# Kernel tuning notes

Hardware: AMD Instinct MI355X
Metric: run time of the kernel (lower is better)

The kernel has to match this reference:

```python
import jax, jax.numpy as jnp
import numpy as np

EMBED_DIM, HIDDEN_DIM, NUM_BINS = 1280, 256, 10

def setup_inputs() -> dict:
    key = jax.random.key(0)
    ks = jax.random.split(key, 7)
    s_in = 1.0 / np.sqrt(EMBED_DIM)
    s_h = 1.0 / np.sqrt(HIDDEN_DIM)
    return {
        "x": jax.random.normal(ks[0], (2, 384, EMBED_DIM), dtype=jnp.float32),
        "Wi": jax.random.uniform(ks[1], (EMBED_DIM, HIDDEN_DIM), jnp.float32, -s_in, s_in),
        "bi": jax.random.uniform(ks[2], (HIDDEN_DIM,), jnp.float32, -s_in, s_in),
        "Wj": jax.random.uniform(ks[3], (EMBED_DIM, HIDDEN_DIM), jnp.float32, -s_in, s_in),
        "bj": jax.random.uniform(ks[4], (HIDDEN_DIM,), jnp.float32, -s_in, s_in),
        "Wo": jax.random.uniform(ks[5], (HIDDEN_DIM, NUM_BINS), jnp.float32, -s_h, s_h),
        "bo": jax.random.uniform(ks[6], (NUM_BINS,), jnp.float32, -s_h, s_h),
    }

def reference(x, Wi, bi, Wj, bj, Wo, bo):
    # x: [B, L, D]
    xi = x @ Wi + bi              # [B, L, H]
    xj = x @ Wj + bj              # [B, L, H]
    pair = xi[:, :, None, :] * xj[:, None, :, :]   # [B, L, L, H]
    h = jax.nn.relu(pair)
    return h @ Wo + bo            # [B, L, L, num_bins]
```

## Files before the change

### kernel.cpp

```cpp
#include <hip/hip_runtime.h>

#define LSEQ 384
#define EMBED 1280
#define HID 256
#define NBINS 10
#define GM 768
#define KP 512

typedef __attribute__((ext_vector_type(8))) short short8;
typedef __attribute__((ext_vector_type(4))) short short4v;
typedef __attribute__((ext_vector_type(4))) float float4v;
typedef __attribute__((ext_vector_type(2))) float float2v;

__device__ __forceinline__ short f2bf(float f) {
    unsigned u = __builtin_bit_cast(unsigned, f);
    u = (u + 0x7fffu + ((u >> 16) & 1u)) >> 16;
    return (short)u;
}

__device__ __forceinline__ void load16_to_lds(const void* g, void* l) {
    __builtin_amdgcn_global_load_lds(
        (const __attribute__((address_space(1))) unsigned int*)g,
        (__attribute__((address_space(3))) unsigned int*)l, 16, 0, 0);
}

__global__ __launch_bounds__(256) void k1_proj_pack(
    const float* __restrict__ x, const float* __restrict__ Wi, const float* __restrict__ bi,
    const float* __restrict__ Wj, const float* __restrict__ bj, const float* __restrict__ Wo,
    short* __restrict__ Aef, short* __restrict__ Bef)
{
    __shared__ short xs[32][32];
    __shared__ short wn[32][32];

    const int tid = threadIdx.x;
    const int m0 = blockIdx.x * 32;
    const int n0 = blockIdx.y * 32;
    const bool isI = (n0 < HID);
    const float* __restrict__ W = isI ? Wi : Wj;
    const int nc0 = n0 & (HID - 1);

    const int lane = tid & 63;
    const int w = tid >> 6;
    const int mh = w >> 1, nh = w & 1;
    const int l15 = lane & 15, q = lane >> 4;

    const int srow = tid >> 3;
    const int sq = (tid & 7) * 4;

    const float* xp = x + (size_t)(m0 + srow) * EMBED + sq;
    const float* wp = W + (size_t)srow * HID + nc0 + sq;

    float4v acc = {0.f, 0.f, 0.f, 0.f};

    for (int ks = 0; ks < EMBED / 32; ++ks) {
        const float4v xv = *(const float4v*)(xp + ks * 32);
        const float4v wv = *(const float4v*)(wp + (size_t)ks * 32 * HID);
        __syncthreads();
        short4v x4;
        x4.x = f2bf(xv.x); x4.y = f2bf(xv.y); x4.z = f2bf(xv.z); x4.w = f2bf(xv.w);
        *(short4v*)&xs[srow][sq] = x4;
        wn[sq + 0][srow] = f2bf(wv.x);
        wn[sq + 1][srow] = f2bf(wv.y);
        wn[sq + 2][srow] = f2bf(wv.z);
        wn[sq + 3][srow] = f2bf(wv.w);
        __syncthreads();
        const short8 a = *(const short8*)&xs[mh * 16 + l15][q * 8];
        const short8 bfr = *(const short8*)&wn[nh * 16 + l15][q * 8];
        acc = __builtin_amdgcn_mfma_f32_16x16x32_bf16(a, bfr, acc, 0, 0, 0);
    }

    const int ncol = n0 + nh * 16 + l15;
    const int mrow0 = m0 + mh * 16;
    if (isI) {
        const int h = ncol;
        float wo[NBINS];
        const float2v* wop = (const float2v*)(Wo + h * NBINS);
#pragma unroll
        for (int c = 0; c < 5; ++c) { float2v t = wop[c]; wo[2 * c] = t.x; wo[2 * c + 1] = t.y; }
        const float bv = bi[h];
#pragma unroll
        for (int r = 0; r < 4; ++r) {
            const int m = mrow0 + q * 4 + r;
            const float v = acc[r] + bv;
            const float p = fmaxf(v, 0.f), pm = fmaxf(-v, 0.f);
            short* ap = Aef + (size_t)m * KP + h;
#pragma unroll
            for (int n = 0; n < NBINS; ++n) {
                ap[(size_t)n * GM * KP]       = f2bf(p  * wo[n]);
                ap[(size_t)n * GM * KP + HID] = f2bf(pm * wo[n]);
            }
        }
    } else {
        const int h = ncol - HID;
        const float bv = bj[h];
#pragma unroll
        for (int r = 0; r < 4; ++r) {
            const int m = mrow0 + q * 4 + r;
            const float v = acc[r] + bv;
            Bef[(size_t)m * KP + h]       = f2bf(fmaxf(v, 0.f));
            Bef[(size_t)m * KP + HID + h] = f2bf(fmaxf(-v, 0.f));
        }
    }
}

__global__ __launch_bounds__(256) void k2_pair_mfma(
    const short* __restrict__ Aef, const short* __restrict__ Bef,
    const float* __restrict__ bo, float* __restrict__ out)
{
    __shared__ __align__(16) char smem[40960];
    short* As = (short*)smem;
    short* Bs = (short*)(smem + 20480);
    float* sout = (float*)smem;

    const int tid = threadIdx.x;
    const int lane = tid & 63;
    const int w = tid >> 6;
    const int ih = w >> 1, jh = w & 1;
    const int l15 = lane & 15, q = lane >> 4;
    const int b = blockIdx.z;
    const int i0 = blockIdx.x * 32, j0 = blockIdx.y * 32;

    const size_t arow0 = (size_t)(b * LSEQ + i0);
    const size_t brow0 = (size_t)(b * LSEQ + j0);
    const int srow = lane >> 2;
    const int skb = (lane & 3) * 8;

    float4v acc[NBINS];
#pragma unroll
    for (int n = 0; n < NBINS; ++n) acc[n] = (float4v){0.f, 0.f, 0.f, 0.f};

    for (int ks = 0; ks < KP / 32; ++ks) {
        const int k0 = ks * 32;
        __syncthreads();
        {
            const int p1 = w, p2 = w + 4;
#pragma unroll
            for (int hh = 0; hh < 2; ++hh) {
                load16_to_lds(Aef + ((size_t)p1 * GM + arow0 + hh * 16 + srow) * KP + k0 + skb,
                              As + p1 * 1024 + hh * 512);
                load16_to_lds(Aef + ((size_t)p2 * GM + arow0 + hh * 16 + srow) * KP + k0 + skb,
                              As + p2 * 1024 + hh * 512);
            }
            if (w < 2) {
                const int p3 = 8 + w;
#pragma unroll
                for (int hh = 0; hh < 2; ++hh)
                    load16_to_lds(Aef + ((size_t)p3 * GM + arow0 + hh * 16 + srow) * KP + k0 + skb,
                                  As + p3 * 1024 + hh * 512);
            } else {
                const int hh = w - 2;
                load16_to_lds(Bef + (brow0 + hh * 16 + srow) * KP + k0 + skb,
                              Bs + hh * 512);
            }
        }
        __syncthreads();
        const short8 bfr = *(const short8*)(Bs + (jh * 16 + l15) * 32 + q * 8);
#pragma unroll
        for (int n = 0; n < NBINS; ++n) {
            const short8 afr = *(const short8*)(As + n * 1024 + (ih * 16 + l15) * 32 + q * 8);
            acc[n] = __builtin_amdgcn_mfma_f32_16x16x32_bf16(afr, bfr, acc[n], 0, 0, 0);
        }
    }
    __syncthreads();

    float bov[NBINS];
    const float2v* bop = (const float2v*)bo;
#pragma unroll
    for (int c = 0; c < 5; ++c) { float2v t = bop[c]; bov[2 * c] = t.x; bov[2 * c + 1] = t.y; }

#pragma unroll
    for (int n = 0; n < NBINS; ++n)
#pragma unroll
        for (int r = 0; r < 4; ++r)
            sout[((ih * 16 + q * 4 + r) * 32 + (jh * 16 + l15)) * NBINS + n] = acc[n][r] + bov[n];
    __syncthreads();

    const float2v* s2 = (const float2v*)sout;
#pragma unroll
    for (int t = 0; t < 20; ++t) {
        const int f = t * 256 + tid;
        const int row = f / 160;
        const int rq = f - row * 160;
        float2v* dst = (float2v*)(out + ((size_t)(b * LSEQ + i0 + row) * LSEQ + j0) * NBINS);
        dst[rq] = s2[f];
    }
}

extern "C" void kernel_launch(void* const* d_in, const int* in_sizes, int n_in,
                              void* d_out, int out_size, void* d_ws, size_t ws_size,
                              hipStream_t stream)
{
    const float* x  = (const float*)d_in[0];
    const float* Wi = (const float*)d_in[1];
    const float* bi = (const float*)d_in[2];
    const float* Wj = (const float*)d_in[3];
    const float* bj = (const float*)d_in[4];
    const float* Wo = (const float*)d_in[5];
    const float* bo = (const float*)d_in[6];
    float* out = (float*)d_out;

    short* Aef = (short*)d_ws;
    short* Bef = Aef + (size_t)NBINS * GM * KP;

    k1_proj_pack<<<dim3(GM / 32, KP / 32), 256, 0, stream>>>(x, Wi, bi, Wj, bj, Wo, Aef, Bef);
    k2_pair_mfma<<<dim3(LSEQ / 32, LSEQ / 32, 2), 256, 0, stream>>>(Aef, Bef, bo, out);
}
```

Baseline: 113.4 us.

## Split projection into prep/gemm/pack kernels and double-buffer pair kernel

Replaces the fused projection kernel with three kernels: a bf16 conversion and transpose of x and the weights, a double-buffered MFMA GEMM using direct global-to-LDS loads, and a pack kernel that writes coalesced, paired bf16 outputs for the Wo-scaled A operand. The pair kernel gains LDS double buffering and a new wave mapping in which each wave reuses its A fragment across two j-halves for five bins. The aim is to remove the scattered strided stores and per-step sync stalls of the old projection and to overlap loads with MFMA in the pair kernel. In exchange it adds two extra kernel launches and global round-trips through workspace buffers, and it uses more LDS per block.

```diff
diff --git a/kernel.cpp b/kernel.cpp
--- a/kernel.cpp
+++ b/kernel.cpp
@@ -12,11 +12,11 @@
 typedef __attribute__((ext_vector_type(4))) float float4v;
 typedef __attribute__((ext_vector_type(2))) float float2v;
 
-__device__ __forceinline__ short f2bf(float f) {
+__device__ __forceinline__ unsigned bfbits(float f) {
     unsigned u = __builtin_bit_cast(unsigned, f);
-    u = (u + 0x7fffu + ((u >> 16) & 1u)) >> 16;
-    return (short)u;
-}
+    return (u + 0x7fffu + ((u >> 16) & 1u)) >> 16;
+}
+__device__ __forceinline__ short f2bf(float f) { return (short)bfbits(f); }
 
 __device__ __forceinline__ void load16_to_lds(const void* g, void* l) {
     __builtin_amdgcn_global_load_lds(
@@ -24,98 +24,126 @@
         (__attribute__((address_space(3))) unsigned int*)l, 16, 0, 0);
 }
 
-__global__ __launch_bounds__(256) void k1_proj_pack(
-    const float* __restrict__ x, const float* __restrict__ Wi, const float* __restrict__ bi,
-    const float* __restrict__ Wj, const float* __restrict__ bj, const float* __restrict__ Wo,
+__global__ __launch_bounds__(256) void k_prep(
+    const float* __restrict__ x, const float* __restrict__ Wi, const float* __restrict__ Wj,
+    short* __restrict__ xb, short* __restrict__ WT)
+{
+    __shared__ float tile[32][33];
+    const int t = threadIdx.x;
+    int bx = blockIdx.x;
+    if (bx < 480) {
+        const int idx = bx * 256 + t;
+        const float4v a = ((const float4v*)x)[idx * 2];
+        const float4v b = ((const float4v*)x)[idx * 2 + 1];
+        short8 o;
+        o[0] = f2bf(a.x); o[1] = f2bf(a.y); o[2] = f2bf(a.z); o[3] = f2bf(a.w);
+        o[4] = f2bf(b.x); o[5] = f2bf(b.y); o[6] = f2bf(b.z); o[7] = f2bf(b.w);
+        ((short8*)xb)[idx] = o;
+    } else {
+        bx -= 480;
+        const int isJ = bx >= 320 ? 1 : 0;
+        if (isJ) bx -= 320;
+        const int tk = bx % 40, tn = bx / 40;
+        const int k0 = tk * 32, n0 = tn * 32;
+        const float* __restrict__ W = isJ ? Wj : Wi;
+        const int r = t >> 3, c4 = (t & 7) * 4;
+        const float4v v = *(const float4v*)(W + (size_t)(k0 + r) * HID + n0 + c4);
+        tile[r][c4 + 0] = v.x; tile[r][c4 + 1] = v.y;
+        tile[r][c4 + 2] = v.z; tile[r][c4 + 3] = v.w;
+        __syncthreads();
+        const int n = r, kc = c4;
+        short4v o;
+        o.x = f2bf(tile[kc + 0][n]); o.y = f2bf(tile[kc + 1][n]);
+        o.z = f2bf(tile[kc + 2][n]); o.w = f2bf(tile[kc + 3][n]);
+        *(short4v*)(WT + (size_t)(isJ * HID + n0 + n) * EMBED + k0 + kc) = o;
+    }
+}
+
+__global__ __launch_bounds__(256) void k_gemm(
+    const short* __restrict__ xb, const short* __restrict__ WT, float* __restrict__ C)
+{
+    __shared__ short As[2][32 * 64];
+    __shared__ short Bs[2][32 * 64];
+    const int tid = threadIdx.x;
+    const int lane = tid & 63, w = tid >> 6;
+    const int mh = w & 1, nh = w >> 1;
+    const int l15 = lane & 15, q = lane >> 4;
+    const int m0 = blockIdx.x * 32, n0 = blockIdx.y * 32;
+    const int lrow = lane >> 3, lcol = (lane & 7) * 8;
+
+    const short* agp = xb + (size_t)(m0 + 8 * w + lrow) * EMBED + lcol;
+    const short* bgp = WT + (size_t)(n0 + 8 * w + lrow) * EMBED + lcol;
+
+    float4v acc = {0.f, 0.f, 0.f, 0.f};
+
+    load16_to_lds(agp, &As[0][w * 512]);
+    load16_to_lds(bgp, &Bs[0][w * 512]);
+    __syncthreads();
+
+    for (int ks = 0; ks < 20; ++ks) {
+        const int cur = ks & 1;
+        if (ks < 19) {
+            load16_to_lds(agp + (ks + 1) * 64, &As[1 - cur][w * 512]);
+            load16_to_lds(bgp + (ks + 1) * 64, &Bs[1 - cur][w * 512]);
+        }
+#pragma unroll
+        for (int kk = 0; kk < 2; ++kk) {
+            const short8 af = *(const short8*)&As[cur][(mh * 16 + l15) * 64 + kk * 32 + q * 8];
+            const short8 bf = *(const short8*)&Bs[cur][(nh * 16 + l15) * 64 + kk * 32 + q * 8];
+            acc = __builtin_amdgcn_mfma_f32_16x16x32_bf16(af, bf, acc, 0, 0, 0);
+        }
+        __syncthreads();
+    }
+
+#pragma unroll
+    for (int r = 0; r < 4; ++r)
+        C[(size_t)(m0 + mh * 16 + q * 4 + r) * KP + n0 + nh * 16 + l15] = acc[r];
+}
+
+__global__ __launch_bounds__(256) void k_pack(
+    const float* __restrict__ C, const float* __restrict__ Wo,
+    const float* __restrict__ bi, const float* __restrict__ bj,
     short* __restrict__ Aef, short* __restrict__ Bef)
 {
-    __shared__ short xs[32][32];
-    __shared__ short wn[32][32];
-
-    const int tid = threadIdx.x;
-    const int m0 = blockIdx.x * 32;
-    const int n0 = blockIdx.y * 32;
-    const bool isI = (n0 < HID);
-    const float* __restrict__ W = isI ? Wi : Wj;
-    const int nc0 = n0 & (HID - 1);
-
-    const int lane = tid & 63;
-    const int w = tid >> 6;
-    const int mh = w >> 1, nh = w & 1;
-    const int l15 = lane & 15, q = lane >> 4;
-
-    const int srow = tid >> 3;
-    const int sq = (tid & 7) * 4;
-
-    const float* xp = x + (size_t)(m0 + srow) * EMBED + sq;
-    const float* wp = W + (size_t)srow * HID + nc0 + sq;
-
-    float4v acc = {0.f, 0.f, 0.f, 0.f};
-
-    for (int ks = 0; ks < EMBED / 32; ++ks) {
-        const float4v xv = *(const float4v*)(xp + ks * 32);
-        const float4v wv = *(const float4v*)(wp + (size_t)ks * 32 * HID);
-        __syncthreads();
-        short4v x4;
-        x4.x = f2bf(xv.x); x4.y = f2bf(xv.y); x4.z = f2bf(xv.z); x4.w = f2bf(xv.w);
-        *(short4v*)&xs[srow][sq] = x4;
-        wn[sq + 0][srow] = f2bf(wv.x);
-        wn[sq + 1][srow] = f2bf(wv.y);
-        wn[sq + 2][srow] = f2bf(wv.z);
-        wn[sq + 3][srow] = f2bf(wv.w);
-        __syncthreads();
-        const short8 a = *(const short8*)&xs[mh * 16 + l15][q * 8];
-        const short8 bfr = *(const short8*)&wn[nh * 16 + l15][q * 8];
-        acc = __builtin_amdgcn_mfma_f32_16x16x32_bf16(a, bfr, acc, 0, 0, 0);
-    }
-
-    const int ncol = n0 + nh * 16 + l15;
-    const int mrow0 = m0 + mh * 16;
-    if (isI) {
-        const int h = ncol;
-        float wo[NBINS];
-        const float2v* wop = (const float2v*)(Wo + h * NBINS);
-#pragma unroll
-        for (int c = 0; c < 5; ++c) { float2v t = wop[c]; wo[2 * c] = t.x; wo[2 * c + 1] = t.y; }
-        const float bv = bi[h];
-#pragma unroll
-        for (int r = 0; r < 4; ++r) {
-            const int m = mrow0 + q * 4 + r;
-            const float v = acc[r] + bv;
-            const float p = fmaxf(v, 0.f), pm = fmaxf(-v, 0.f);
-            short* ap = Aef + (size_t)m * KP + h;
-#pragma unroll
-            for (int n = 0; n < NBINS; ++n) {
-                ap[(size_t)n * GM * KP]       = f2bf(p  * wo[n]);
-                ap[(size_t)n * GM * KP + HID] = f2bf(pm * wo[n]);
-            }
-        }
-    } else {
-        const int h = ncol - HID;
-        const float bv = bj[h];
-#pragma unroll
-        for (int r = 0; r < 4; ++r) {
-            const int m = mrow0 + q * 4 + r;
-            const float v = acc[r] + bv;
-            Bef[(size_t)m * KP + h]       = f2bf(fmaxf(v, 0.f));
-            Bef[(size_t)m * KP + HID + h] = f2bf(fmaxf(-v, 0.f));
-        }
-    }
-}
-
-__global__ __launch_bounds__(256) void k2_pair_mfma(
+    __shared__ float xrow[HID];
+    __shared__ float woL[NBINS * HID];
+    const int t = threadIdx.x, m = blockIdx.x;
+
+    xrow[t] = C[(size_t)m * KP + t] + bi[t];
+#pragma unroll
+    for (int c = 0; c < NBINS; ++c) woL[c * HID + t] = Wo[(size_t)t * NBINS + c];
+
+    const float vj = C[(size_t)m * KP + HID + t] + bj[t];
+    Bef[(size_t)m * KP + t]       = f2bf(fmaxf(vj, 0.f));
+    Bef[(size_t)m * KP + HID + t] = f2bf(fmaxf(-vj, 0.f));
+    __syncthreads();
+
+    const int k = 2 * t;
+    const int h = k & (HID - 1);
+    float v0, v1;
+    if (t < 128) { v0 = fmaxf(xrow[h], 0.f);  v1 = fmaxf(xrow[h + 1], 0.f); }
+    else         { v0 = fmaxf(-xrow[h], 0.f); v1 = fmaxf(-xrow[h + 1], 0.f); }
+
+#pragma unroll
+    for (int n = 0; n < NBINS; ++n) {
+        const unsigned lo = bfbits(v0 * woL[n * HID + h]);
+        const unsigned hi = bfbits(v1 * woL[n * HID + h + 1]);
+        ((unsigned*)(Aef + ((size_t)n * GM + m) * KP))[t] = (hi << 16) | lo;
+    }
+}
+
+__global__ __launch_bounds__(256) void k2_pair(
     const short* __restrict__ Aef, const short* __restrict__ Bef,
     const float* __restrict__ bo, float* __restrict__ out)
 {
-    __shared__ __align__(16) char smem[40960];
+    __shared__ __align__(16) char smem[45056];
     short* As = (short*)smem;
-    short* Bs = (short*)(smem + 20480);
+    short* Bs = (short*)(smem + 40960);
     float* sout = (float*)smem;
 
     const int tid = threadIdx.x;
-    const int lane = tid & 63;
-    const int w = tid >> 6;
-    const int ih = w >> 1, jh = w & 1;
+    const int lane = tid & 63, w = tid >> 6;
+    const int ih = w & 1, nb = (w >> 1) * 5;
     const int l15 = lane & 15, q = lane >> 4;
     const int b = blockIdx.z;
     const int i0 = blockIdx.x * 32, j0 = blockIdx.y * 32;
@@ -125,54 +153,69 @@
     const int srow = lane >> 2;
     const int skb = (lane & 3) * 8;
 
-    float4v acc[NBINS];
-#pragma unroll
-    for (int n = 0; n < NBINS; ++n) acc[n] = (float4v){0.f, 0.f, 0.f, 0.f};
-
-    for (int ks = 0; ks < KP / 32; ++ks) {
-        const int k0 = ks * 32;
-        __syncthreads();
-        {
-            const int p1 = w, p2 = w + 4;
-#pragma unroll
-            for (int hh = 0; hh < 2; ++hh) {
-                load16_to_lds(Aef + ((size_t)p1 * GM + arow0 + hh * 16 + srow) * KP + k0 + skb,
-                              As + p1 * 1024 + hh * 512);
-                load16_to_lds(Aef + ((size_t)p2 * GM + arow0 + hh * 16 + srow) * KP + k0 + skb,
-                              As + p2 * 1024 + hh * 512);
-            }
-            if (w < 2) {
-                const int p3 = 8 + w;
-#pragma unroll
-                for (int hh = 0; hh < 2; ++hh)
-                    load16_to_lds(Aef + ((size_t)p3 * GM + arow0 + hh * 16 + srow) * KP + k0 + skb,
-                                  As + p3 * 1024 + hh * 512);
-            } else {
-                const int hh = w - 2;
-                load16_to_lds(Bef + (brow0 + hh * 16 + srow) * KP + k0 + skb,
-                              Bs + hh * 512);
-            }
+    float4v acc[2][5];
+#pragma unroll
+    for (int jh = 0; jh < 2; ++jh)
+#pragma unroll
+        for (int nn = 0; nn < 5; ++nn) acc[jh][nn] = (float4v){0.f, 0.f, 0.f, 0.f};
+
+#define STAGE_K2(ks, buf)                                                               \
+    {                                                                                   \
+        const int k0_ = (ks) * 32;                                                      \
+        short* AsB = As + (buf) * 10240;                                                \
+        short* BsB = Bs + (buf) * 1024;                                                 \
+        const int p1 = w, p2 = w + 4;                                                   \
+        _Pragma("unroll")                                                               \
+        for (int hh = 0; hh < 2; ++hh) {                                                \
+            load16_to_lds(Aef + ((size_t)p1 * GM + arow0 + hh * 16 + srow) * KP + k0_ + skb, \
+                          AsB + p1 * 1024 + hh * 512);                                  \
+            load16_to_lds(Aef + ((size_t)p2 * GM + arow0 + hh * 16 + srow) * KP + k0_ + skb, \
+                          AsB + p2 * 1024 + hh * 512);                                  \
+        }                                                                               \
+        if (w < 2) {                                                                    \
+            const int p3 = 8 + w;                                                       \
+            _Pragma("unroll")                                                           \
+            for (int hh = 0; hh < 2; ++hh)                                              \
+                load16_to_lds(Aef + ((size_t)p3 * GM + arow0 + hh * 16 + srow) * KP + k0_ + skb, \
+                              AsB + p3 * 1024 + hh * 512);                              \
+        } else {                                                                        \
+            load16_to_lds(Bef + (brow0 + (w - 2) * 16 + srow) * KP + k0_ + skb,         \
+                          BsB + (w - 2) * 512);                                         \
+        }                                                                               \
+    }
+
+    STAGE_K2(0, 0)
+    __syncthreads();
+
+    for (int ks = 0; ks < 16; ++ks) {
+        const int cur = ks & 1;
+        if (ks < 15) STAGE_K2(ks + 1, 1 - cur)
+        const short* AsB = As + cur * 10240;
+        const short* BsB = Bs + cur * 1024;
+        const short8 bfr0 = *(const short8*)(BsB + (0 * 16 + l15) * 32 + q * 8);
+        const short8 bfr1 = *(const short8*)(BsB + (1 * 16 + l15) * 32 + q * 8);
+#pragma unroll
+        for (int nn = 0; nn < 5; ++nn) {
+            const short8 afr = *(const short8*)(AsB + (nb + nn) * 1024 + (ih * 16 + l15) * 32 + q * 8);
+            acc[0][nn] = __builtin_amdgcn_mfma_f32_16x16x32_bf16(afr, bfr0, acc[0][nn], 0, 0, 0);
+            acc[1][nn] = __builtin_amdgcn_mfma_f32_16x16x32_bf16(afr, bfr1, acc[1][nn], 0, 0, 0);
         }
         __syncthreads();
-        const short8 bfr = *(const short8*)(Bs + (jh * 16 + l15) * 32 + q * 8);
-#pragma unroll
-        for (int n = 0; n < NBINS; ++n) {
-            const short8 afr = *(const short8*)(As + n * 1024 + (ih * 16 + l15) * 32 + q * 8);
-            acc[n] = __builtin_amdgcn_mfma_f32_16x16x32_bf16(afr, bfr, acc[n], 0, 0, 0);
-        }
-    }
-    __syncthreads();
+    }
 
     float bov[NBINS];
     const float2v* bop = (const float2v*)bo;
 #pragma unroll
-    for (int c = 0; c < 5; ++c) { float2v t = bop[c]; bov[2 * c] = t.x; bov[2 * c + 1] = t.y; }
-
-#pragma unroll
-    for (int n = 0; n < NBINS; ++n)
-#pragma unroll
-        for (int r = 0; r < 4; ++r)
-            sout[((ih * 16 + q * 4 + r) * 32 + (jh * 16 + l15)) * NBINS + n] = acc[n][r] + bov[n];
+    for (int c = 0; c < 5; ++c) { float2v tv = bop[c]; bov[2 * c] = tv.x; bov[2 * c + 1] = tv.y; }
+
+#pragma unroll
+    for (int jh = 0; jh < 2; ++jh)
+#pragma unroll
+        for (int nn = 0; nn < 5; ++nn)
+#pragma unroll
+            for (int r = 0; r < 4; ++r)
+                sout[((ih * 16 + q * 4 + r) * 32 + (jh * 16 + l15)) * NBINS + nb + nn] =
+                    acc[jh][nn][r] + bov[nb + nn];
     __syncthreads();
 
     const float2v* s2 = (const float2v*)sout;
@@ -199,9 +242,15 @@
     const float* bo = (const float*)d_in[6];
     float* out = (float*)d_out;
 
-    short* Aef = (short*)d_ws;
-    short* Bef = Aef + (size_t)NBINS * GM * KP;
-
-    k1_proj_pack<<<dim3(GM / 32, KP / 32), 256, 0, stream>>>(x, Wi, bi, Wj, bj, Wo, Aef, Bef);
-    k2_pair_mfma<<<dim3(LSEQ / 32, LSEQ / 32, 2), 256, 0, stream>>>(Aef, Bef, bo, out);
-}
+    char* p = (char*)d_ws;
+    float* C   = (float*)p;                 p += (size_t)GM * KP * 4;
+    short* xb  = (short*)p;                 p += (size_t)GM * EMBED * 2;
+    short* WT  = (short*)p;                 p += (size_t)KP * EMBED * 2;
+    short* Aef = (short*)p;                 p += (size_t)NBINS * GM * KP * 2;
+    short* Bef = (short*)p;
+
+    k_prep<<<1120, 256, 0, stream>>>(x, Wi, Wj, xb, WT);
+    k_gemm<<<dim3(GM / 32, KP / 32), 256, 0, stream>>>(xb, WT, C);
+    k_pack<<<GM, 256, 0, stream>>>(C, Wo, bi, bj, Aef, Bef);
+    k2_pair<<<dim3(LSEQ / 32, LSEQ / 32, 2), 256, 0, stream>>>(Aef, Bef, bo, out);
+}
```

Measured after the change: 107.5 us. 5.2% less time.
